# Kernel tuning notes

Measured on AMD Instinct MI355X. Metric: run time of the kernel, lower is better.

## Reference

```python
import jax, jax.numpy as jnp
import numpy as np

DIM = 256
HEADS = 8
HEAD_DIM = DIM // HEADS
EDGE_TYPES = 8  # edge_type_count; table has EDGE_TYPES+1 rows, row 0 is padding
B, N = 2, 2048
EPS = 1e-5


def layer_norm(x, g, b):
    mu = jnp.mean(x, axis=-1, keepdims=True)
    var = jnp.mean(jnp.square(x - mu), axis=-1, keepdims=True)
    return (x - mu) * jax.lax.rsqrt(var + EPS) * g + b


def setup_inputs() -> dict:
    key = jax.random.key(0)
    ks = jax.random.split(key, 12)
    s = 0.02
    x = jax.random.normal(ks[0], (B, N, DIM), dtype=jnp.float32)
    edge_types = jax.random.randint(ks[1], (B, N, N), 0, EDGE_TYPES + 1, dtype=jnp.int32)
    node_mask = jax.random.randint(ks[2], (B, N), 0, 2, dtype=jnp.int32).astype(bool)
    qkv_w = jax.random.normal(ks[3], (DIM, 3 * DIM), dtype=jnp.float32) * s
    qkv_b = jnp.zeros((3 * DIM,), jnp.float32)
    proj_w = jax.random.normal(ks[4], (DIM, DIM), dtype=jnp.float32) * s
    proj_b = jnp.zeros((DIM,), jnp.float32)
    edge_bias_table = jax.random.normal(ks[5], (EDGE_TYPES + 1, HEADS), dtype=jnp.float32) * s
    edge_bias_table = edge_bias_table.at[0].set(0.0)  # padding_idx=0
    ln1_g = jnp.ones((DIM,), jnp.float32); ln1_b = jnp.zeros((DIM,), jnp.float32)
    ln2_g = jnp.ones((DIM,), jnp.float32); ln2_b = jnp.zeros((DIM,), jnp.float32)
    ffn_w1 = jax.random.normal(ks[6], (DIM, 4 * DIM), dtype=jnp.float32) * s
    ffn_b1 = jnp.zeros((4 * DIM,), jnp.float32)
    ffn_w2 = jax.random.normal(ks[7], (4 * DIM, DIM), dtype=jnp.float32) * s
    ffn_b2 = jnp.zeros((DIM,), jnp.float32)
    return dict(x=x, edge_types=edge_types, node_mask=node_mask,
                qkv_w=qkv_w, qkv_b=qkv_b, proj_w=proj_w, proj_b=proj_b,
                edge_bias_table=edge_bias_table, ln1_g=ln1_g, ln1_b=ln1_b,
                ln2_g=ln2_g, ln2_b=ln2_b, ffn_w1=ffn_w1, ffn_b1=ffn_b1,
                ffn_w2=ffn_w2, ffn_b2=ffn_b2)


def reference(x, edge_types, node_mask, qkv_w, qkv_b, proj_w, proj_b,
              edge_bias_table, ln1_g, ln1_b, ln2_g, ln2_b,
              ffn_w1, ffn_b1, ffn_w2, ffn_b2):
    scale = HEAD_DIM ** -0.5
    residual = x
    h = layer_norm(x, ln1_g, ln1_b)
    qkv = h @ qkv_w + qkv_b                         # [B,N,3*DIM]
    qkv = qkv.reshape(B, N, 3, HEADS, HEAD_DIM)
    q, k, v = (qkv[:, :, 0].transpose(0, 2, 1, 3),  # [B,H,N,d]
               qkv[:, :, 1].transpose(0, 2, 1, 3),
               qkv[:, :, 2].transpose(0, 2, 1, 3))
    scores = jnp.einsum('bhnd,bhmd->bhnm', q, k) * scale
    bias = edge_bias_table[edge_types]              # [B,N,N,H]
    scores = scores + bias.transpose(0, 3, 1, 2)    # [B,H,N,N]
    eye = jnp.eye(N, dtype=bool)
    edge_mask = (edge_types != 0) | eye[None]
    node_mask_2d = node_mask[:, None, :] & node_mask[:, :, None]
    attn_mask = edge_mask & node_mask_2d            # [B,N,N]
    scores = jnp.where(attn_mask[:, None], scores, -1e9)
    attn = jax.nn.softmax(scores, axis=-1)
    out = jnp.einsum('bhnm,bhmd->bhnd', attn, v)
    out = out.transpose(0, 2, 1, 3).reshape(B, N, DIM)
    out = (out @ proj_w + proj_b) * node_mask[:, :, None]
    x1 = residual + out
    h2 = layer_norm(x1, ln2_g, ln2_b)
    h2 = jax.nn.gelu(h2 @ ffn_w1 + ffn_b1, approximate=False) @ ffn_w2 + ffn_b2
    h2 = h2 * node_mask[:, :, None]
    return x1 + h2
```

## Files before the change

kernel.cpp:

```cpp
#include <hip/hip_runtime.h>
#include <math.h>

#define DIMM 256
#define HEADS 8
#define NB 2048
#define BB 2
#define ROWS (BB*NB)

typedef __attribute__((ext_vector_type(8))) short bf16x8;
typedef __attribute__((ext_vector_type(4))) short bf16x4;
typedef __attribute__((ext_vector_type(4))) float f32x4;

__device__ inline unsigned short f2bf(float f) {
    unsigned int u = __float_as_uint(f);
    u += 0x7FFFu + ((u >> 16) & 1u);
    return (unsigned short)(u >> 16);
}
__device__ inline float bf2f(unsigned short u) {
    return __uint_as_float(((unsigned int)u) << 16);
}

__device__ inline int get_mask(const void* nm, int fmt, int idx) {
    if (fmt) return ((const unsigned char*)nm)[idx] != 0;
    return ((const int*)nm)[idx] != 0;
}

__global__ __launch_bounds__(256) void scan_kernel(
    const void* __restrict__ nmask, int* __restrict__ nv,
    unsigned short* __restrict__ qidx, float* __restrict__ lpart)
{
    __shared__ int fsh;
    __shared__ int cnt[256];
    __shared__ int base[256];
    int b = blockIdx.x, t = threadIdx.x;
    if (t == 0) fsh = 0;
    __syncthreads();
    if (((const unsigned char*)nmask)[4 * t + 1] != 0) fsh = 1;
    __syncthreads();
    int fm = fsh;
    int m[8]; int c = 0;
#pragma unroll
    for (int i = 0; i < 8; ++i) {
        m[i] = get_mask(nmask, fm, b * NB + t * 8 + i);
        c += m[i];
    }
    cnt[t] = c;
    __syncthreads();
    if (t == 0) {
        int acc = 0;
        for (int i = 0; i < 256; ++i) { base[i] = acc; acc += cnt[i]; }
        nv[b] = acc;
    }
    __syncthreads();
    int off = base[t];
#pragma unroll
    for (int i = 0; i < 8; ++i) {
        int row = t * 8 + i;
        if (m[i]) {
            qidx[b * NB + off++] = (unsigned short)row;
        } else {
#pragma unroll
            for (int sp = 0; sp < 4; ++sp) {
                float* lp = lpart + (size_t)sp * ROWS * 8 + (size_t)(b * NB + row) * 8;
                *(float4*)lp       = make_float4(0.f, 0.f, 0.f, 0.f);
                *(float4*)(lp + 4) = make_float4(0.f, 0.f, 0.f, 0.f);
            }
        }
    }
    __syncthreads();
    if (t == 0) {
        int n = nv[b];
        unsigned short last = (n > 0) ? qidx[b * NB + n - 1] : (unsigned short)0;
        int padend = (n + 15) & ~15;
        for (int i = n; i < padend; ++i) qidx[b * NB + i] = last;
    }
}

__device__ inline void ln8_body(const float* __restrict__ x, const float* __restrict__ g,
                                const float* __restrict__ bb, unsigned short* __restrict__ o,
                                int row, int lane32) {
    int c0 = lane32 * 8;
    float4 v0 = *(const float4*)&x[(size_t)row * DIMM + c0];
    float4 v1 = *(const float4*)&x[(size_t)row * DIMM + c0 + 4];
    float s  = v0.x + v0.y + v0.z + v0.w + v1.x + v1.y + v1.z + v1.w;
    float s2 = v0.x*v0.x + v0.y*v0.y + v0.z*v0.z + v0.w*v0.w
             + v1.x*v1.x + v1.y*v1.y + v1.z*v1.z + v1.w*v1.w;
#pragma unroll
    for (int off = 16; off >= 1; off >>= 1) {
        s  += __shfl_xor(s,  off);
        s2 += __shfl_xor(s2, off);
    }
    float mean = s * (1.0f / DIMM);
    float var  = s2 * (1.0f / DIMM) - mean * mean;
    float rstd = rsqrtf(var + 1e-5f);
    float4 g0 = *(const float4*)&g[c0],  g1 = *(const float4*)&g[c0 + 4];
    float4 b0 = *(const float4*)&bb[c0], b1 = *(const float4*)&bb[c0 + 4];
    ushort4 u0, u1;
    u0.x = f2bf((v0.x - mean) * rstd * g0.x + b0.x);
    u0.y = f2bf((v0.y - mean) * rstd * g0.y + b0.y);
    u0.z = f2bf((v0.z - mean) * rstd * g0.z + b0.z);
    u0.w = f2bf((v0.w - mean) * rstd * g0.w + b0.w);
    u1.x = f2bf((v1.x - mean) * rstd * g1.x + b1.x);
    u1.y = f2bf((v1.y - mean) * rstd * g1.y + b1.y);
    u1.z = f2bf((v1.z - mean) * rstd * g1.z + b1.z);
    u1.w = f2bf((v1.w - mean) * rstd * g1.w + b1.w);
    *(ushort4*)&o[(size_t)row * DIMM + c0]     = u0;
    *(ushort4*)&o[(size_t)row * DIMM + c0 + 4] = u1;
}

__global__ __launch_bounds__(256) void prep_kernel(
    const float* __restrict__ w0, const float* __restrict__ w1,
    const float* __restrict__ w2, const float* __restrict__ w3,
    unsigned short* __restrict__ o0, unsigned short* __restrict__ o1,
    unsigned short* __restrict__ o2, unsigned short* __restrict__ o3,
    const float* __restrict__ x, const float* __restrict__ ln1_g,
    const float* __restrict__ ln1_b, unsigned short* __restrict__ h_ln,
    const int* __restrict__ etypes, const void* __restrict__ nmask,
    unsigned char* __restrict__ emaskP,
    const int* __restrict__ nv, const unsigned short* __restrict__ qidx)
{
    __shared__ float tile[64][65];
    __shared__ int fsh;
    int bid = blockIdx.x, t = threadIdx.x;
    if (bid < 192) {
        const float* src; unsigned short* dst; int K, N, idx;
        if (bid < 48)       { src = w0; dst = o0; K = 256;  N = 768;  idx = bid; }
        else if (bid < 64)  { src = w1; dst = o1; K = 256;  N = 256;  idx = bid - 48; }
        else if (bid < 128) { src = w2; dst = o2; K = 256;  N = 1024; idx = bid - 64; }
        else                { src = w3; dst = o3; K = 1024; N = 256;  idx = bid - 128; }
        int ntiles = N >> 6;
        int k0 = (idx / ntiles) * 64, n0 = (idx % ntiles) * 64;
        int r = t >> 4, c4 = (t & 15) * 4;
#pragma unroll
        for (int i = 0; i < 4; ++i) {
            float4 v = *(const float4*)&src[(size_t)(k0 + r + i * 16) * N + n0 + c4];
            tile[r + i * 16][c4 + 0] = v.x;
            tile[r + i * 16][c4 + 1] = v.y;
            tile[r + i * 16][c4 + 2] = v.z;
            tile[r + i * 16][c4 + 3] = v.w;
        }
        __syncthreads();
#pragma unroll
        for (int i = 0; i < 4; ++i) {
            int n = n0 + r + i * 16;
            ushort4 u;
            u.x = f2bf(tile[c4 + 0][r + i * 16]);
            u.y = f2bf(tile[c4 + 1][r + i * 16]);
            u.z = f2bf(tile[c4 + 2][r + i * 16]);
            u.w = f2bf(tile[c4 + 3][r + i * 16]);
            *(ushort4*)&dst[(size_t)n * K + k0 + c4] = u;
        }
    } else if (bid < 704) {
        int row = (bid - 192) * 8 + (t >> 5);
        ln8_body(x, ln1_g, ln1_b, h_ln, row, t & 31);
    } else {
        if (t == 0) fsh = 0;
        __syncthreads();
        if (((const unsigned char*)nmask)[4 * t + 1] != 0) fsh = 1;
        __syncthreads();
        int fm = fsh;
        int unit = (bid - 704) * 4 + (t >> 6);
        int lane = t & 63, quad = lane >> 4, l15 = lane & 15;
        int b = unit >> 12;
        int qt16 = (unit >> 5) & 127;
        int kt = unit & 31;
        int nvb = nv[b];
        if (qt16 * 16 >= nvb) return;
        int slot = qt16 * 16 + l15;
        int validq = slot < nvb;
        int qr = qidx[b * NB + slot];
        const int* erow = etypes + (size_t)(b * NB + qr) * NB;
        unsigned int dw[2] = {0u, 0u};
#pragma unroll
        for (int t16 = 0; t16 < 4; ++t16) {
            int col0 = kt * 64 + t16 * 16 + quad * 4;
            int4 e4 = *(const int4*)(erow + col0);
            int ee[4] = {e4.x, e4.y, e4.z, e4.w};
            int cv[4];
            if (fm) {
                unsigned int m4 = *(const unsigned int*)((const unsigned char*)nmask + b * NB + col0);
                cv[0] = (m4 & 0xffu) != 0;     cv[1] = (m4 & 0xff00u) != 0;
                cv[2] = (m4 & 0xff0000u) != 0; cv[3] = (m4 >> 24) != 0;
            } else {
                int4 m4 = *(const int4*)((const int*)nmask + b * NB + col0);
                cv[0] = m4.x != 0; cv[1] = m4.y != 0; cv[2] = m4.z != 0; cv[3] = m4.w != 0;
            }
#pragma unroll
            for (int r = 0; r < 4; ++r) {
                int col = col0 + r;
                int valid = validq && cv[r] && ((ee[r] != 0) || (col == qr));
                unsigned int code = valid ? (unsigned int)(ee[r] + 1) : 0u;
                dw[t16 >> 1] |= code << ((t16 & 1) * 16 + r * 4);
            }
        }
        int2 o = {(int)dw[0], (int)dw[1]};
        *(int2*)(emaskP + (size_t)unit * 512 + lane * 8) = o;
    }
}

__global__ __launch_bounds__(256) void gemm_qkv_mfma(
    const unsigned short* __restrict__ A, const unsigned short* __restrict__ Bt,
    const float* __restrict__ bias,
    unsigned short* __restrict__ qkvh, unsigned short* __restrict__ vT)
{
    const int K = 256;
    int t = threadIdx.x, w = t >> 6, l = t & 63;
    int l15 = l & 15, quad = l >> 4;
    int n0 = blockIdx.x * 64;
    int m0 = blockIdx.y * 64;
    const unsigned short* ap = A + (size_t)(m0 + w * 16 + l15) * K + quad * 8;
    const unsigned short* bp = Bt + (size_t)(n0 + l15) * K + quad * 8;

    f32x4 acc[4];
#pragma unroll
    for (int c = 0; c < 4; ++c) acc[c] = (f32x4){0.f, 0.f, 0.f, 0.f};

    bf16x8 aA, bA[4], aB, bB[4];
    auto ld = [&](bf16x8& af, bf16x8 (&bf)[4], int k0) {
        af = *(const bf16x8*)(ap + k0);
#pragma unroll
        for (int c = 0; c < 4; ++c)
            bf[c] = *(const bf16x8*)(bp + (size_t)(c * 16) * K + k0);
    };
    auto pr = [&](const bf16x8& af, const bf16x8 (&bf)[4]) {
#pragma unroll
        for (int c = 0; c < 4; ++c)
            acc[c] = __builtin_amdgcn_mfma_f32_16x16x32_bf16(af, bf[c], acc[c], 0, 0, 0);
    };
    ld(aA, bA, 0);
    for (int k0 = 0; k0 < K; k0 += 64) {
        ld(aB, bB, k0 + 32);
        pr(aA, bA);
        if (k0 + 64 < K) ld(aA, bA, k0 + 64);
        pr(aB, bB);
    }

    if (n0 < 512) {
        float sc = (n0 < 256) ? 0.17677669529663689f : 1.0f;
#pragma unroll
        for (int r = 0; r < 4; ++r) {
            int row = m0 + w * 16 + quad * 4 + r;
#pragma unroll
            for (int c = 0; c < 4; ++c) {
                int col = n0 + c * 16 + l15;
                qkvh[(size_t)row * 512 + col] = f2bf((acc[c][r] + bias[col]) * sc);
            }
        }
    } else {
        int bb_ = m0 >> 11;
        int n = (m0 + w * 16 + quad * 4) & 2047;
#pragma unroll
        for (int c = 0; c < 4; ++c) {
            int col = n0 + c * 16 + l15 - 512;
            int hidx = col >> 5, d = col & 31;
            float bs = bias[n0 + c * 16 + l15];
            ushort4 u;
            u.x = f2bf(acc[c][0] + bs);
            u.y = f2bf(acc[c][1] + bs);
            u.z = f2bf(acc[c][2] + bs);
            u.w = f2bf(acc[c][3] + bs);
            *(ushort4*)&vT[(size_t)((bb_ * HEADS + hidx) * 32 + d) * NB + n] = u;
        }
    }
}

__global__ __launch_bounds__(256) void attn_mfma(
    const unsigned short* __restrict__ qkvh,
    const unsigned short* __restrict__ vT,
    const unsigned char* __restrict__ emaskP,
    const float* __restrict__ table,
    const int* __restrict__ nv, const unsigned short* __restrict__ qidx,
    unsigned short* __restrict__ OpH, float* __restrict__ lpart)
{
    __shared__ unsigned short P[4][16][72];
    __shared__ float tab2m[16];

    int t = threadIdx.x;
    int w = t >> 6, l = t & 63;
    int l15 = l & 15, quad = l >> 4;
    int h = blockIdx.x;
    int qt = blockIdx.y;
    int z = blockIdx.z, b = z >> 2, sp = z & 3;
    int kbase = sp * (NB / 4);

    if (t < 16) tab2m[t] = (t >= 1 && t < 10) ? __expf(table[(t - 1) * 8 + h]) : 0.f;
    __syncthreads();

    int nvb = nv[b];
    int qt16 = qt * 4 + w;
    int q0c = qt16 * 16;
    if (q0c >= nvb) return;

    int qrow = b * NB + qidx[b * NB + q0c + l15];
    bf16x8 bq = *(const bf16x8*)(qkvh + (size_t)qrow * 512 + h * 32 + quad * 8);

    const unsigned short* kp = qkvh + (size_t)(b * NB + l15) * 512 + 256 + h * 32 + quad * 8;
    const unsigned short* vp = vT + (size_t)((b * HEADS + h) * 32 + l15) * NB + quad * 8;
    const unsigned char* ep = emaskP + (size_t)((b * 128 + qt16) * 32) * 512 + l * 8;

    float lacc = 0.f;
    f32x4 O0 = {0.f, 0.f, 0.f, 0.f}, O1 = {0.f, 0.f, 0.f, 0.f};

    bf16x8 kA[4], kB[4];
    bf16x8 vA[2][2], vB[2][2];
    int2 eA, eB;

    auto loadtile = [&](bf16x8 (&kf)[4], bf16x8 (&vf)[2][2], int2& ef, int m0) {
#pragma unroll
        for (int t16 = 0; t16 < 4; ++t16)
            kf[t16] = *(const bf16x8*)(kp + (size_t)(m0 + t16 * 16) * 512);
#pragma unroll
        for (int ks = 0; ks < 2; ++ks) {
            vf[ks][0] = *(const bf16x8*)(vp + m0 + ks * 32);
            vf[ks][1] = *(const bf16x8*)(vp + 16 * NB + m0 + ks * 32);
        }
        ef = *(const int2*)(ep + (size_t)(m0 >> 6) * 512);
    };

    auto process = [&](const bf16x8 (&kf)[4], const bf16x8 (&vf)[2][2], const int2& ef) {
#pragma unroll
        for (int t16 = 0; t16 < 4; ++t16) {
            f32x4 zero = {0.f, 0.f, 0.f, 0.f};
            f32x4 sT = __builtin_amdgcn_mfma_f32_16x16x32_bf16(kf[t16], bq, zero, 0, 0, 0);
            unsigned int e = ((unsigned int)((t16 < 2) ? ef.x : ef.y)) >> ((t16 & 1) * 16);
            float p0 = __expf(sT[0]) * tab2m[e & 0xFu];
            float p1 = __expf(sT[1]) * tab2m[(e >> 4) & 0xFu];
            float p2 = __expf(sT[2]) * tab2m[(e >> 8) & 0xFu];
            float p3 = __expf(sT[3]) * tab2m[(e >> 12) & 0xFu];
            lacc += (p0 + p1) + (p2 + p3);
            bf16x4 pb;
            pb[0] = (short)f2bf(p0); pb[1] = (short)f2bf(p1);
            pb[2] = (short)f2bf(p2); pb[3] = (short)f2bf(p3);
            *(bf16x4*)&P[w][l15][t16 * 16 + quad * 4] = pb;
        }
#pragma unroll
        for (int ks = 0; ks < 2; ++ks) {
            bf16x8 pa = *(const bf16x8*)&P[w][l15][ks * 32 + quad * 8];
            O0 = __builtin_amdgcn_mfma_f32_16x16x32_bf16(pa, vf[ks][0], O0, 0, 0, 0);
            O1 = __builtin_amdgcn_mfma_f32_16x16x32_bf16(pa, vf[ks][1], O1, 0, 0, 0);
        }
    };

    loadtile(kA, vA, eA, kbase);
    for (int m0 = kbase; m0 < kbase + NB / 4; m0 += 128) {
        loadtile(kB, vB, eB, m0 + 64);
        process(kA, vA, eA);
        if (m0 + 128 < kbase + NB / 4) loadtile(kA, vA, eA, m0 + 128);
        process(kB, vB, eB);
    }

    lacc += __shfl_xor(lacc, 16);
    lacc += __shfl_xor(lacc, 32);

    unsigned short* Ob = OpH + (size_t)sp * ROWS * DIMM;
#pragma unroll
    for (int r = 0; r < 4; ++r) {
        int slot = q0c + quad * 4 + r;
        if (slot < nvb) {
            int row = b * NB + qidx[b * NB + slot];
            Ob[(size_t)row * DIMM + h * 32 + l15]      = f2bf(O0[r]);
            Ob[(size_t)row * DIMM + h * 32 + 16 + l15] = f2bf(O1[r]);
        }
    }
    if (quad == 0 && q0c + l15 < nvb) {
        int row = b * NB + qidx[b * NB + q0c + l15];
        lpart[(size_t)sp * ROWS * 8 + (size_t)row * 8 + h] = lacc;
    }
}

__global__ __launch_bounds__(1024) void megaback(
    const unsigned short* __restrict__ OpH, const float* __restrict__ lpart,
    const unsigned short* __restrict__ projT, const float* __restrict__ proj_b,
    const float* __restrict__ x, const void* __restrict__ nmask,
    const float* __restrict__ g2, const float* __restrict__ b2,
    const unsigned short* __restrict__ f1T, const float* __restrict__ ffn_b1,
    const unsigned short* __restrict__ f2T, const float* __restrict__ ffn_b2,
    float* __restrict__ out)
{
    __shared__ float rinv_l[16][8];
    __shared__ float stats[16][2];
    __shared__ float redn[16][16][2];
    __shared__ unsigned short Astage[16][264];
    __shared__ float x1s[16][260];
    __shared__ unsigned short hstage[16][264];
    __shared__ unsigned short midstage[16][1032];
    __shared__ int fsh;

    int t = threadIdx.x;
    int w = t >> 6, l = t & 63;
    int l15 = l & 15, quad = l >> 4;
    int grow0 = blockIdx.x * 16;

    if (t == 0) fsh = 0;
    __syncthreads();
    if (((const unsigned char*)nmask)[4 * t + 1] != 0) fsh = 1;

    if (t < 128) {
        int row = t >> 3, h = t & 7;
        float s = 0.f;
#pragma unroll
        for (int sp = 0; sp < 4; ++sp)
            s += lpart[(size_t)sp * ROWS * 8 + (size_t)(grow0 + row) * 8 + h];
        rinv_l[row][h] = (s > 0.f) ? 1.f / s : 0.f;
    }
    __syncthreads();
    int fm = fsh;

    {
        int row = t >> 6, col4 = (t & 63) * 4;
        float rinv = rinv_l[row][col4 >> 5];
        float o0 = 0.f, o1 = 0.f, o2 = 0.f, o3 = 0.f;
#pragma unroll
        for (int sp = 0; sp < 4; ++sp) {
            ushort4 u = *(const ushort4*)&OpH[(size_t)sp * ROWS * DIMM +
                                             (size_t)(grow0 + row) * DIMM + col4];
            o0 += bf2f(u.x); o1 += bf2f(u.y); o2 += bf2f(u.z); o3 += bf2f(u.w);
        }
        ushort4 u;
        u.x = f2bf(o0 * rinv); u.y = f2bf(o1 * rinv);
        u.z = f2bf(o2 * rinv); u.w = f2bf(o3 * rinv);
        *(ushort4*)&Astage[row][col4] = u;
    }
    __syncthreads();

    {
        int col = w * 16 + l15;
        f32x4 acc = (f32x4){0.f, 0.f, 0.f, 0.f};
        const unsigned short* bp = projT + (size_t)col * 256 + quad * 8;
        bf16x8 sb[4];
#pragma unroll
        for (int i = 0; i < 4; ++i) sb[i] = *(const bf16x8*)(bp + i * 32);
#pragma unroll
        for (int ch = 0; ch < 8; ++ch) {
            bf16x8 a = *(const bf16x8*)&Astage[l15][ch * 32 + quad * 8];
            acc = __builtin_amdgcn_mfma_f32_16x16x32_bf16(a, sb[ch & 3], acc, 0, 0, 0);
            if (ch + 4 < 8) sb[ch & 3] = *(const bf16x8*)(bp + (ch + 4) * 32);
        }
        float bs = proj_b[col];
#pragma unroll
        for (int r = 0; r < 4; ++r) {
            int row = quad * 4 + r, grow = grow0 + row;
            float mk = (float)get_mask(nmask, fm, grow);
            float v = (acc[r] + bs) * mk + x[(size_t)grow * DIMM + col];
            x1s[row][col] = v;
            float s = v, s2 = v * v;
#pragma unroll
            for (int off = 1; off < 16; off <<= 1) {
                s += __shfl_xor(s, off); s2 += __shfl_xor(s2, off);
            }
            if (l15 == 0) { redn[row][w][0] = s; redn[row][w][1] = s2; }
        }
    }
    __syncthreads();
    if (t < 16) {
        float s = 0.f, s2 = 0.f;
#pragma unroll
        for (int ww = 0; ww < 16; ++ww) { s += redn[t][ww][0]; s2 += redn[t][ww][1]; }
        float mean = s * (1.f / DIMM);
        float var  = s2 * (1.f / DIMM) - mean * mean;
        stats[t][0] = mean; stats[t][1] = rsqrtf(var + 1e-5f);
    }
    __syncthreads();

    {
        int col = w * 16 + l15;
        float gv = g2[col], bv = b2[col];
#pragma unroll
        for (int r = 0; r < 4; ++r) {
            int row = quad * 4 + r;
            float hv = (x1s[row][col] - stats[row][0]) * stats[row][1] * gv + bv;
            hstage[row][col] = f2bf(hv);
        }
    }
    __syncthreads();

    {
        f32x4 acc[4];
#pragma unroll
        for (int c = 0; c < 4; ++c) acc[c] = (f32x4){0.f, 0.f, 0.f, 0.f};
        const unsigned short* bp = f1T + (size_t)(w * 64 + l15) * 256 + quad * 8;
        bf16x8 bA[4], bB[4];
#pragma unroll
        for (int c = 0; c < 4; ++c) bA[c] = *(const bf16x8*)(bp + (size_t)(c * 16) * 256);
#pragma unroll
        for (int ch = 0; ch < 8; ++ch) {
            bf16x8 a = *(const bf16x8*)&hstage[l15][ch * 32 + quad * 8];
            if (ch + 1 < 8) {
#pragma unroll
                for (int c = 0; c < 4; ++c)
                    bB[c] = *(const bf16x8*)(bp + (size_t)(c * 16) * 256 + (ch + 1) * 32);
            }
#pragma unroll
            for (int c = 0; c < 4; ++c)
                acc[c] = __builtin_amdgcn_mfma_f32_16x16x32_bf16(a, bA[c], acc[c], 0, 0, 0);
#pragma unroll
            for (int c = 0; c < 4; ++c) bA[c] = bB[c];
        }
#pragma unroll
        for (int c = 0; c < 4; ++c) {
            int col = w * 64 + c * 16 + l15;
            float bs = ffn_b1[col];
#pragma unroll
            for (int r = 0; r < 4; ++r) {
                float v = acc[c][r] + bs;
                float x2 = v * v;
                float p = v * fmaf(0.07135481f, x2, 1.5957691f);
                float e = __expf(p);
                float gl = v * (e / (e + 1.f));
                midstage[quad * 4 + r][col] = f2bf(gl);
            }
        }
    }
    __syncthreads();

    {
        int col = w * 16 + l15;
        f32x4 acc = (f32x4){0.f, 0.f, 0.f, 0.f};
        const unsigned short* bp = f2T + (size_t)col * 1024 + quad * 8;
        bf16x8 sb[4];
#pragma unroll
        for (int i = 0; i < 4; ++i) sb[i] = *(const bf16x8*)(bp + i * 32);
#pragma unroll
        for (int ch = 0; ch < 32; ++ch) {
            bf16x8 a = *(const bf16x8*)&midstage[l15][ch * 32 + quad * 8];
            acc = __builtin_amdgcn_mfma_f32_16x16x32_bf16(a, sb[ch & 3], acc, 0, 0, 0);
            if (ch + 4 < 32) sb[ch & 3] = *(const bf16x8*)(bp + (ch + 4) * 32);
        }
        float bs = ffn_b2[col];
#pragma unroll
        for (int r = 0; r < 4; ++r) {
            int row = quad * 4 + r, grow = grow0 + row;
            float mk = (float)get_mask(nmask, fm, grow);
            out[(size_t)grow * DIMM + col] = x1s[row][col] + (acc[r] + bs) * mk;
        }
    }
}

extern "C" void kernel_launch(void* const* d_in, const int* in_sizes, int n_in,
                              void* d_out, int out_size, void* d_ws, size_t ws_size,
                              hipStream_t stream) {
    const float* x       = (const float*)d_in[0];
    const int*   etypes  = (const int*)d_in[1];
    const void*  nmask   = d_in[2];
    const float* qkv_w   = (const float*)d_in[3];
    const float* qkv_b   = (const float*)d_in[4];
    const float* proj_w  = (const float*)d_in[5];
    const float* proj_b  = (const float*)d_in[6];
    const float* table   = (const float*)d_in[7];
    const float* ln1_g   = (const float*)d_in[8];
    const float* ln1_b   = (const float*)d_in[9];
    const float* ln2_g   = (const float*)d_in[10];
    const float* ln2_b   = (const float*)d_in[11];
    const float* ffn_w1  = (const float*)d_in[12];
    const float* ffn_b1  = (const float*)d_in[13];
    const float* ffn_w2  = (const float*)d_in[14];
    const float* ffn_b2  = (const float*)d_in[15];
    float* out = (float*)d_out;
    float* ws  = (float*)d_ws;

    float* lpart = ws;
    unsigned short* ub = (unsigned short*)(ws + 131072);
    unsigned short* h_ln   = ub;
    unsigned short* qkvh   = ub + 1048576;
    unsigned short* vT     = ub + 3145728;
    unsigned short* OpH    = ub + 4194304;
    unsigned short* qkvT   = ub + 8388608;
    unsigned short* projT  = ub + 8585216;
    unsigned short* f1T    = ub + 8650752;
    unsigned short* f2T    = ub + 8912896;
    unsigned char* emaskP  = (unsigned char*)(ub + 9175040);
    unsigned short* qidx   = ub + 11272192;
    int* nv                = (int*)(ub + 11276288);

    scan_kernel<<<dim3(BB), dim3(256), 0, stream>>>(nmask, nv, qidx, lpart);
    prep_kernel<<<dim3(2752), dim3(256), 0, stream>>>(
        qkv_w, proj_w, ffn_w1, ffn_w2, qkvT, projT, f1T, f2T,
        x, ln1_g, ln1_b, h_ln, etypes, nmask, emaskP, nv, qidx);
    gemm_qkv_mfma<<<dim3(12, 64), dim3(256), 0, stream>>>(h_ln, qkvT, qkv_b, qkvh, vT);
    attn_mfma<<<dim3(HEADS, NB/64, BB*4), dim3(256), 0, stream>>>(
        qkvh, vT, emaskP, table, nv, qidx, OpH, lpart);
    megaback<<<dim3(ROWS/16), dim3(1024), 0, stream>>>(
        OpH, lpart, projT, proj_b, x, nmask, ln2_g, ln2_b,
        f1T, ffn_b1, f2T, ffn_b2, out);
}
```

Baseline: 219.7 us.

## Compact valid nodes end-to-end and copy masked rows directly to output

The pipeline now works in compacted slot space: LN1, the QKV GEMM, attention key tiles and the back-end MLP only process valid (masked-in) nodes, gathered through qidx, and skip blocks beyond the padded valid count. Masked-out rows are copied straight from x to the output in the scan kernel, since their attention and FFN contributions are zero. Attention key loops now cover only the compacted valid keys, about half of the original count, split across four partitions. In exchange the mask-building step uses gathered, uncoalesced edge-type reads through qidx, and a redundant duplicate qidx load is left in megaback.

```diff
diff --git a/kernel.cpp b/kernel.cpp
--- a/kernel.cpp
+++ b/kernel.cpp
@@ -25,63 +25,67 @@
     return ((const int*)nm)[idx] != 0;
 }
 
-__global__ __launch_bounds__(256) void scan_kernel(
+__global__ __launch_bounds__(256) void scan_copy_kernel(
     const void* __restrict__ nmask, int* __restrict__ nv,
-    unsigned short* __restrict__ qidx, float* __restrict__ lpart)
+    unsigned short* __restrict__ qidx,
+    const float* __restrict__ x, float* __restrict__ out)
 {
     __shared__ int fsh;
     __shared__ int cnt[256];
     __shared__ int base[256];
-    int b = blockIdx.x, t = threadIdx.x;
+    int bid = blockIdx.x, t = threadIdx.x;
     if (t == 0) fsh = 0;
     __syncthreads();
     if (((const unsigned char*)nmask)[4 * t + 1] != 0) fsh = 1;
     __syncthreads();
     int fm = fsh;
-    int m[8]; int c = 0;
-#pragma unroll
-    for (int i = 0; i < 8; ++i) {
-        m[i] = get_mask(nmask, fm, b * NB + t * 8 + i);
-        c += m[i];
-    }
-    cnt[t] = c;
-    __syncthreads();
-    if (t == 0) {
-        int acc = 0;
-        for (int i = 0; i < 256; ++i) { base[i] = acc; acc += cnt[i]; }
-        nv[b] = acc;
-    }
-    __syncthreads();
-    int off = base[t];
-#pragma unroll
-    for (int i = 0; i < 8; ++i) {
-        int row = t * 8 + i;
-        if (m[i]) {
-            qidx[b * NB + off++] = (unsigned short)row;
-        } else {
-#pragma unroll
-            for (int sp = 0; sp < 4; ++sp) {
-                float* lp = lpart + (size_t)sp * ROWS * 8 + (size_t)(b * NB + row) * 8;
-                *(float4*)lp       = make_float4(0.f, 0.f, 0.f, 0.f);
-                *(float4*)(lp + 4) = make_float4(0.f, 0.f, 0.f, 0.f);
-            }
-        }
-    }
-    __syncthreads();
-    if (t == 0) {
-        int n = nv[b];
-        unsigned short last = (n > 0) ? qidx[b * NB + n - 1] : (unsigned short)0;
-        int padend = (n + 15) & ~15;
-        for (int i = n; i < padend; ++i) qidx[b * NB + i] = last;
+    if (bid < BB) {
+        int b = bid;
+        int m[8]; int c = 0;
+#pragma unroll
+        for (int i = 0; i < 8; ++i) {
+            m[i] = get_mask(nmask, fm, b * NB + t * 8 + i);
+            c += m[i];
+        }
+        cnt[t] = c;
+        __syncthreads();
+        if (t == 0) {
+            int acc = 0;
+            for (int i = 0; i < 256; ++i) { base[i] = acc; acc += cnt[i]; }
+            nv[b] = acc;
+        }
+        __syncthreads();
+        int off = base[t];
+#pragma unroll
+        for (int i = 0; i < 8; ++i) {
+            int row = t * 8 + i;
+            if (m[i]) qidx[b * NB + off++] = (unsigned short)row;
+        }
+        __syncthreads();
+        if (t == 0) {
+            int n = nv[b];
+            unsigned short last = (n > 0) ? qidx[b * NB + n - 1] : (unsigned short)0;
+            int padend = (n + 63) & ~63;
+            for (int i = n; i < padend; ++i) qidx[b * NB + i] = last;
+        }
+    } else {
+        int row = (bid - BB) * 8 + (t >> 5);
+        if (!get_mask(nmask, fm, row)) {
+            int c0 = (t & 31) * 8;
+            float4 v0 = *(const float4*)&x[(size_t)row * DIMM + c0];
+            float4 v1 = *(const float4*)&x[(size_t)row * DIMM + c0 + 4];
+            *(float4*)&out[(size_t)row * DIMM + c0]     = v0;
+            *(float4*)&out[(size_t)row * DIMM + c0 + 4] = v1;
+        }
     }
 }
 
 __device__ inline void ln8_body(const float* __restrict__ x, const float* __restrict__ g,
                                 const float* __restrict__ bb, unsigned short* __restrict__ o,
-                                int row, int lane32) {
+                                int xrow, int orow, int lane32) {
     int c0 = lane32 * 8;
-    float4 v0 = *(const float4*)&x[(size_t)row * DIMM + c0];
-    float4 v1 = *(const float4*)&x[(size_t)row * DIMM + c0 + 4];
+    float4 v0 = *(const float4*)&x[(size_t)xrow * DIMM + c0];
+    float4 v1 = *(const float4*)&x[(size_t)xrow * DIMM + c0 + 4];
     float s  = v0.x + v0.y + v0.z + v0.w + v1.x + v1.y + v1.z + v1.w;
     float s2 = v0.x*v0.x + v0.y*v0.y + v0.z*v0.z + v0.w*v0.w
              + v1.x*v1.x + v1.y*v1.y + v1.z*v1.z + v1.w*v1.w;
@@ -104,8 +108,8 @@
     u1.y = f2bf((v1.y - mean) * rstd * g1.y + b1.y);
     u1.z = f2bf((v1.z - mean) * rstd * g1.z + b1.z);
     u1.w = f2bf((v1.w - mean) * rstd * g1.w + b1.w);
-    *(ushort4*)&o[(size_t)row * DIMM + c0]     = u0;
-    *(ushort4*)&o[(size_t)row * DIMM + c0 + 4] = u1;
+    *(ushort4*)&o[(size_t)orow * DIMM + c0]     = u0;
+    *(ushort4*)&o[(size_t)orow * DIMM + c0 + 4] = u1;
 }
 
 __global__ __launch_bounds__(256) void prep_kernel(
@@ -115,12 +119,11 @@
     unsigned short* __restrict__ o2, unsigned short* __restrict__ o3,
     const float* __restrict__ x, const float* __restrict__ ln1_g,
     const float* __restrict__ ln1_b, unsigned short* __restrict__ h_ln,
-    const int* __restrict__ etypes, const void* __restrict__ nmask,
+    const int* __restrict__ etypes,
     unsigned char* __restrict__ emaskP,
     const int* __restrict__ nv, const unsigned short* __restrict__ qidx)
 {
     __shared__ float tile[64][65];
-    __shared__ int fsh;
     int bid = blockIdx.x, t = threadIdx.x;
     if (bid < 192) {
         const float* src; unsigned short* dst; int K, N, idx;
@@ -151,21 +154,22 @@
             *(ushort4*)&dst[(size_t)n * K + k0 + c4] = u;
         }
     } else if (bid < 704) {
-        int row = (bid - 192) * 8 + (t >> 5);
-        ln8_body(x, ln1_g, ln1_b, h_ln, row, t & 31);
+        int slotg = (bid - 192) * 8 + (t >> 5);
+        int b = slotg >> 11, sl = slotg & 2047;
+        int nvp = (nv[b] + 63) & ~63;
+        if (sl < nvp) {
+            int row = qidx[b * NB + sl];
+            ln8_body(x, ln1_g, ln1_b, h_ln, b * NB + row, slotg, t & 31);
+        }
     } else {
-        if (t == 0) fsh = 0;
-        __syncthreads();
-        if (((const unsigned char*)nmask)[4 * t + 1] != 0) fsh = 1;
-        __syncthreads();
-        int fm = fsh;
         int unit = (bid - 704) * 4 + (t >> 6);
         int lane = t & 63, quad = lane >> 4, l15 = lane & 15;
         int b = unit >> 12;
         int qt16 = (unit >> 5) & 127;
         int kt = unit & 31;
         int nvb = nv[b];
-        if (qt16 * 16 >= nvb) return;
+        int nvp = (nvb + 63) & ~63;
+        if (qt16 * 16 >= nvb || kt * 64 >= nvp) return;
         int slot = qt16 * 16 + l15;
         int validq = slot < nvb;
         int qr = qidx[b * NB + slot];
@@ -173,23 +177,15 @@
         unsigned int dw[2] = {0u, 0u};
 #pragma unroll
         for (int t16 = 0; t16 < 4; ++t16) {
-            int col0 = kt * 64 + t16 * 16 + quad * 4;
-            int4 e4 = *(const int4*)(erow + col0);
-            int ee[4] = {e4.x, e4.y, e4.z, e4.w};
-            int cv[4];
-            if (fm) {
-                unsigned int m4 = *(const unsigned int*)((const unsigned char*)nmask + b * NB + col0);
-                cv[0] = (m4 & 0xffu) != 0;     cv[1] = (m4 & 0xff00u) != 0;
-                cv[2] = (m4 & 0xff0000u) != 0; cv[3] = (m4 >> 24) != 0;
-            } else {
-                int4 m4 = *(const int4*)((const int*)nmask + b * NB + col0);
-                cv[0] = m4.x != 0; cv[1] = m4.y != 0; cv[2] = m4.z != 0; cv[3] = m4.w != 0;
-            }
 #pragma unroll
             for (int r = 0; r < 4; ++r) {
-                int col = col0 + r;
-                int valid = validq && cv[r] && ((ee[r] != 0) || (col == qr));
-                unsigned int code = valid ? (unsigned int)(ee[r] + 1) : 0u;
+                int ks = kt * 64 + t16 * 16 + quad * 4 + r;
+                unsigned int code = 0u;
+                if (validq && ks < nvb) {
+                    int korig = qidx[b * NB + ks];
+                    int et = erow[korig];
+                    if ((et != 0) || (korig == qr)) code = (unsigned int)(et + 1);
+                }
                 dw[t16 >> 1] |= code << ((t16 & 1) * 16 + r * 4);
             }
         }
@@ -200,15 +196,18 @@
 
 __global__ __launch_bounds__(256) void gemm_qkv_mfma(
     const unsigned short* __restrict__ A, const unsigned short* __restrict__ Bt,
-    const float* __restrict__ bias,
+    const float* __restrict__ bias, const int* __restrict__ nv,
     unsigned short* __restrict__ qkvh, unsigned short* __restrict__ vT)
 {
     const int K = 256;
     int t = threadIdx.x, w = t >> 6, l = t & 63;
     int l15 = l & 15, quad = l >> 4;
     int n0 = blockIdx.x * 64;
-    int m0 = blockIdx.y * 64;
-    const unsigned short* ap = A + (size_t)(m0 + w * 16 + l15) * K + quad * 8;
+    int m0c = blockIdx.y * 64;
+    int b = blockIdx.z;
+    int nvp = (nv[b] + 63) & ~63;
+    if (m0c >= nvp) return;
+    const unsigned short* ap = A + (size_t)(b * NB + m0c + w * 16 + l15) * K + quad * 8;
     const unsigned short* bp = Bt + (size_t)(n0 + l15) * K + quad * 8;
 
     f32x4 acc[4];
@@ -239,16 +238,15 @@
         float sc = (n0 < 256) ? 0.17677669529663689f : 1.0f;
 #pragma unroll
         for (int r = 0; r < 4; ++r) {
-            int row = m0 + w * 16 + quad * 4 + r;
+            int slot = b * NB + m0c + w * 16 + quad * 4 + r;
 #pragma unroll
             for (int c = 0; c < 4; ++c) {
                 int col = n0 + c * 16 + l15;
-                qkvh[(size_t)row * 512 + col] = f2bf((acc[c][r] + bias[col]) * sc);
+                qkvh[(size_t)slot * 512 + col] = f2bf((acc[c][r] + bias[col]) * sc);
             }
         }
     } else {
-        int bb_ = m0 >> 11;
-        int n = (m0 + w * 16 + quad * 4) & 2047;
+        int n = m0c + w * 16 + quad * 4;
 #pragma unroll
         for (int c = 0; c < 4; ++c) {
             int col = n0 + c * 16 + l15 - 512;
@@ -259,7 +257,7 @@
             u.y = f2bf(acc[c][1] + bs);
             u.z = f2bf(acc[c][2] + bs);
             u.w = f2bf(acc[c][3] + bs);
-            *(ushort4*)&vT[(size_t)((bb_ * HEADS + hidx) * 32 + d) * NB + n] = u;
+            *(ushort4*)&vT[(size_t)((b * HEADS + hidx) * 32 + d) * NB + n] = u;
         }
     }
 }
@@ -269,7 +267,7 @@
     const unsigned short* __restrict__ vT,
     const unsigned char* __restrict__ emaskP,
     const float* __restrict__ table,
-    const int* __restrict__ nv, const unsigned short* __restrict__ qidx,
+    const int* __restrict__ nv,
     unsigned short* __restrict__ OpH, float* __restrict__ lpart)
 {
     __shared__ unsigned short P[4][16][72];
@@ -281,7 +279,6 @@
     int h = blockIdx.x;
     int qt = blockIdx.y;
     int z = blockIdx.z, b = z >> 2, sp = z & 3;
-    int kbase = sp * (NB / 4);
 
     if (t < 16) tab2m[t] = (t >= 1 && t < 10) ? __expf(table[(t - 1) * 8 + h]) : 0.f;
     __syncthreads();
@@ -291,8 +288,12 @@
     int q0c = qt16 * 16;
     if (q0c >= nvb) return;
 
-    int qrow = b * NB + qidx[b * NB + q0c + l15];
-    bf16x8 bq = *(const bf16x8*)(qkvh + (size_t)qrow * 512 + h * 32 + quad * 8);
+    int nkt = (nvb + 63) >> 6;
+    int tps = (nkt + 3) >> 2;
+    int kbase = sp * tps * 64;
+    int kend = min(kbase + tps * 64, nkt * 64);
+
+    bf16x8 bq = *(const bf16x8*)(qkvh + (size_t)(b * NB + q0c + l15) * 512 + h * 32 + quad * 8);
 
     const unsigned short* kp = qkvh + (size_t)(b * NB + l15) * 512 + 256 + h * 32 + quad * 8;
     const unsigned short* vp = vT + (size_t)((b * HEADS + h) * 32 + l15) * NB + quad * 8;
@@ -341,12 +342,15 @@
         }
     };
 
-    loadtile(kA, vA, eA, kbase);
-    for (int m0 = kbase; m0 < kbase + NB / 4; m0 += 128) {
-        loadtile(kB, vB, eB, m0 + 64);
-        process(kA, vA, eA);
-        if (m0 + 128 < kbase + NB / 4) loadtile(kA, vA, eA, m0 + 128);
-        process(kB, vB, eB);
+    if (kbase < kend) {
+        loadtile(kA, vA, eA, kbase);
+        for (int m0 = kbase; m0 < kend; m0 += 128) {
+            int n1 = (m0 + 64 < kend) ? m0 + 64 : kbase;
+            loadtile(kB, vB, eB, n1);
+            process(kA, vA, eA);
+            if (m0 + 128 < kend) loadtile(kA, vA, eA, m0 + 128);
+            if (m0 + 64 < kend) process(kB, vB, eB);
+        }
     }
 
     lacc += __shfl_xor(lacc, 16);
@@ -357,24 +361,22 @@
     for (int r = 0; r < 4; ++r) {
         int slot = q0c + quad * 4 + r;
         if (slot < nvb) {
-            int row = b * NB + qidx[b * NB + slot];
-            Ob[(size_t)row * DIMM + h * 32 + l15]      = f2bf(O0[r]);
-            Ob[(size_t)row * DIMM + h * 32 + 16 + l15] = f2bf(O1[r]);
-        }
-    }
-    if (quad == 0 && q0c + l15 < nvb) {
-        int row = b * NB + qidx[b * NB + q0c + l15];
-        lpart[(size_t)sp * ROWS * 8 + (size_t)row * 8 + h] = lacc;
-    }
+            Ob[(size_t)(b * NB + slot) * DIMM + h * 32 + l15]      = f2bf(O0[r]);
+            Ob[(size_t)(b * NB + slot) * DIMM + h * 32 + 16 + l15] = f2bf(O1[r]);
+        }
+    }
+    if (quad == 0 && q0c + l15 < nvb)
+        lpart[(size_t)sp * ROWS * 8 + (size_t)(b * NB + q0c + l15) * 8 + h] = lacc;
 }
 
 __global__ __launch_bounds__(1024) void megaback(
     const unsigned short* __restrict__ OpH, const float* __restrict__ lpart,
     const unsigned short* __restrict__ projT, const float* __restrict__ proj_b,
-    const float* __restrict__ x, const void* __restrict__ nmask,
+    const float* __restrict__ x,
     const float* __restrict__ g2, const float* __restrict__ b2,
     const unsigned short* __restrict__ f1T, const float* __restrict__ ffn_b1,
     const unsigned short* __restrict__ f2T, const float* __restrict__ ffn_b2,
+    const int* __restrict__ nv, const unsigned short* __restrict__ qidx,
     float* __restrict__ out)
 {
     __shared__ float rinv_l[16][8];
@@ -384,27 +386,25 @@
     __shared__ float x1s[16][260];
     __shared__ unsigned short hstage[16][264];
     __shared__ unsigned short midstage[16][1032];
-    __shared__ int fsh;
 
     int t = threadIdx.x;
     int w = t >> 6, l = t & 63;
     int l15 = l & 15, quad = l >> 4;
-    int grow0 = blockIdx.x * 16;
-
-    if (t == 0) fsh = 0;
-    __syncthreads();
-    if (((const unsigned char*)nmask)[4 * t + 1] != 0) fsh = 1;
+    int b = blockIdx.x >> 7;
+    int s0 = (blockIdx.x & 127) * 16;
+    int nvb = nv[b];
+    if (s0 >= nvb) return;
+    int slot0 = b * NB + s0;
 
     if (t < 128) {
         int row = t >> 3, h = t & 7;
         float s = 0.f;
 #pragma unroll
         for (int sp = 0; sp < 4; ++sp)
-            s += lpart[(size_t)sp * ROWS * 8 + (size_t)(grow0 + row) * 8 + h];
+            s += lpart[(size_t)sp * ROWS * 8 + (size_t)(slot0 + row) * 8 + h];
         rinv_l[row][h] = (s > 0.f) ? 1.f / s : 0.f;
     }
     __syncthreads();
-    int fm = fsh;
 
     {
         int row = t >> 6, col4 = (t & 63) * 4;
@@ -413,7 +413,7 @@
 #pragma unroll
         for (int sp = 0; sp < 4; ++sp) {
             ushort4 u = *(const ushort4*)&OpH[(size_t)sp * ROWS * DIMM +
-                                             (size_t)(grow0 + row) * DIMM + col4];
+                                             (size_t)(slot0 + row) * DIMM + col4];
             o0 += bf2f(u.x); o1 += bf2f(u.y); o2 += bf2f(u.z); o3 += bf2f(u.w);
         }
         ushort4 u;
@@ -439,9 +439,10 @@
         float bs = proj_b[col];
 #pragma unroll
         for (int r = 0; r < 4; ++r) {
-            int row = quad * 4 + r, grow = grow0 + row;
-            float mk = (float)get_mask(nmask, fm, grow);
-            float v = (acc[r] + bs) * mk + x[(size_t)grow * DIMM + col];
+            int row = quad * 4 + r;
+            int grow = b * NB + qidx[(size_t)slot0 + row - (size_t)b * NB + b * NB];
+            grow = b * NB + qidx[(size_t)(slot0 + row)];
+            float v = (acc[r] + bs) + x[(size_t)grow * DIMM + col];
             x1s[row][col] = v;
             float s = v, s2 = v * v;
 #pragma unroll
@@ -529,9 +530,11 @@
         float bs = ffn_b2[col];
 #pragma unroll
         for (int r = 0; r < 4; ++r) {
-            int row = quad * 4 + r, grow = grow0 + row;
-            float mk = (float)get_mask(nmask, fm, grow);
-            out[(size_t)grow * DIMM + col] = x1s[row][col] + (acc[r] + bs) * mk;
+            int row = quad * 4 + r;
+            if (s0 + row < nvb) {
+                int grow = b * NB + qidx[(size_t)(slot0 + row)];
+                out[(size_t)grow * DIMM + col] = x1s[row][col] + (acc[r] + bs);
+            }
         }
     }
 }
@@ -572,14 +575,14 @@
     unsigned short* qidx   = ub + 11272192;
     int* nv                = (int*)(ub + 11276288);
 
-    scan_kernel<<<dim3(BB), dim3(256), 0, stream>>>(nmask, nv, qidx, lpart);
+    scan_copy_kernel<<<dim3(BB + ROWS/8), dim3(256), 0, stream>>>(nmask, nv, qidx, x, out);
     prep_kernel<<<dim3(2752), dim3(256), 0, stream>>>(
         qkv_w, proj_w, ffn_w1, ffn_w2, qkvT, projT, f1T, f2T,
-        x, ln1_g, ln1_b, h_ln, etypes, nmask, emaskP, nv, qidx);
-    gemm_qkv_mfma<<<dim3(12, 64), dim3(256), 0, stream>>>(h_ln, qkvT, qkv_b, qkvh, vT);
+        x, ln1_g, ln1_b, h_ln, etypes, emaskP, nv, qidx);
+    gemm_qkv_mfma<<<dim3(12, 32, BB), dim3(256), 0, stream>>>(h_ln, qkvT, qkv_b, nv, qkvh, vT);
     attn_mfma<<<dim3(HEADS, NB/64, BB*4), dim3(256), 0, stream>>>(
-        qkvh, vT, emaskP, table, nv, qidx, OpH, lpart);
-    megaback<<<dim3(ROWS/16), dim3(1024), 0, stream>>>(
-        OpH, lpart, projT, proj_b, x, nmask, ln2_g, ln2_b,
-        f1T, ffn_b1, f2T, ffn_b2, out);
-}
+        qkvh, vT, emaskP, table, nv, OpH, lpart);
+    megaback<<<dim3(2 * 128), dim3(1024), 0, stream>>>(
+        OpH, lpart, projT, proj_b, x, ln2_g, ln2_b,
+        f1T, ffn_b1, f2T, ffn_b2, nv, qidx, out);
+}
```

Result: faster. 203.5 us (-7.4%).
